# Kernel optimization log

Measured on AMD Instinct MI355X. Metric: run time of the kernel, lower is better.

The kernel has to match this reference:

```python
import jax, jax.numpy as jnp
import numpy as np

N_HEADS = 8
D_MODEL = 128
EPS = 1e-6


def setup_inputs() -> dict:
    key = jax.random.key(0)
    k1, k2, k3, k4, k5 = jax.random.split(key, 5)
    B, Dim, F, T = 1, D_MODEL, 256, 1024
    queries = jax.random.normal(k1, (B, Dim, F, T), dtype=jnp.float32)
    keys = jax.random.normal(k2, (B, Dim, F, T), dtype=jnp.float32)
    values = jax.random.normal(k3, (B, Dim, F, T), dtype=jnp.float32)
    # out_projection: Linear(d_model, d_output) with d_output == d_model
    W_out = jax.random.normal(k4, (D_MODEL, D_MODEL), dtype=jnp.float32) / np.sqrt(D_MODEL)
    b_out = jax.random.normal(k5, (D_MODEL,), dtype=jnp.float32) * 0.01
    return {"queries": queries, "keys": keys, "values": values,
            "W_out": W_out, "b_out": b_out}


def _to_heads(x, B, Dim, L, H):
    # (B, Dim, F, T) -> (B, L, Dim) -> (B, L, H, d) -> (B, H, L, d)
    return x.reshape(B, Dim, L).transpose(0, 2, 1).reshape(B, L, H, Dim // H).transpose(0, 2, 1, 3)


def reference(queries, keys, values, W_out, b_out):
    B, Dim, F, T = queries.shape
    L = F * T
    H = N_HEADS
    q = jax.nn.sigmoid(_to_heads(queries, B, Dim, L, H))  # (B,H,L,d)
    k = jax.nn.sigmoid(_to_heads(keys, B, Dim, L, H))
    v = _to_heads(values, B, Dim, L, H)

    # NOTE: sums are over the HEAD axis (dim=1), faithful to the original code
    ks = k.sum(axis=1, keepdims=True)                      # (B,1,L,d)
    qs = q.sum(axis=1, keepdims=True)
    sink_incoming = 1.0 / jnp.sum((q + EPS) * (ks + EPS), axis=-1)      # (B,H,L)
    source_outgoing = 1.0 / jnp.sum((k + EPS) * (qs + EPS), axis=-1)    # (B,H,L)
    conserved_sink = jnp.sum(
        (q + EPS) * ((k * source_outgoing[..., None]).sum(axis=1, keepdims=True) + EPS),
        axis=-1)                                                        # (B,H,L)
    conserved_source = jnp.sum(
        (k + EPS) * ((q * sink_incoming[..., None]).sum(axis=1, keepdims=True) + EPS),
        axis=-1)
    conserved_source = jnp.clip(conserved_source, -1.0, 1.0)
    sink_allocation = jax.nn.sigmoid(conserved_sink * (float(L) / float(L)))
    source_competition = jax.nn.softmax(conserved_source, axis=-1) * float(L)

    kv = jnp.einsum('bhld,bhlm->bhdm', k, v * source_competition[..., None])
    qkv = jnp.einsum('bhld,bhdm->bhlm', q * sink_incoming[..., None], kv)
    x = (qkv * sink_allocation[..., None]).transpose(0, 2, 1, 3).reshape(B, L, Dim)
    x = x @ W_out.T + b_out                                 # dropout is identity (eval)
    return x.transpose(0, 2, 1).reshape(B, Dim, F, T)
```

## Files before the change

kernel.cpp:

```cpp
#include <hip/hip_runtime.h>
#include <hip/hip_bf16.h>

#define L_TOT (1 << 18)
#define L_SHIFT 18
#define NHEAD 8
#define DHEAD 16
#define DMODEL 128
#define EPSF 1e-6f

typedef float f32x4 __attribute__((ext_vector_type(4)));
typedef short bf16x8 __attribute__((ext_vector_type(8)));

__device__ __forceinline__ float frcp(float x) { return __builtin_amdgcn_rcpf(x); }
__device__ __forceinline__ float sigm(float x) { return frcp(1.0f + __expf(-x)); }
__device__ __forceinline__ unsigned short f2bf(float f) {
    return (unsigned short)((__float_as_uint(f) + 0x8000u) >> 16);
}

__device__ __forceinline__ float qsum(float x) {
    x += __int_as_float(__builtin_amdgcn_update_dpp(0, __float_as_int(x), 0xB1, 0xf, 0xf, true));
    x += __int_as_float(__builtin_amdgcn_update_dpp(0, __float_as_int(x), 0x4E, 0xf, 0xf, true));
    return x;
}

__global__ __launch_bounds__(256) void k1_stats(
        const float* __restrict__ Q, const float* __restrict__ K,
        float* __restrict__ scale_o, float* __restrict__ wbuf,
        float* __restrict__ sep) {
    __shared__ float hredl[4][8];

    const int t = threadIdx.x;
    const int l0 = blockIdx.x * 64;
    const int c = t >> 2;
    const int s = t & 3;
    const int l = l0 + c;

    float qv[32], kv[32];
#pragma unroll
    for (int h = 0; h < 8; ++h)
#pragma unroll
        for (int r = 0; r < 4; ++r) {
            const int p = h * 16 + s * 4 + r;
            qv[h * 4 + r] = Q[(p << L_SHIFT) + l];
            kv[h * 4 + r] = K[(p << L_SHIFT) + l];
        }

    unsigned a[32];
#pragma unroll
    for (int i = 0; i < 32; ++i) {
        const unsigned qu = __float_as_uint(sigm(qv[i])) + 0x8000u;
        const unsigned ku = __float_as_uint(sigm(kv[i])) + 0x8000u;
        a[i] = (ku & 0xffff0000u) | (qu >> 16);
    }

    float ks[4] = {0.f, 0.f, 0.f, 0.f}, qs[4] = {0.f, 0.f, 0.f, 0.f};
#pragma unroll
    for (int h = 0; h < 8; ++h)
#pragma unroll
        for (int j = 0; j < 4; ++j) {
            const unsigned u = a[h * 4 + j];
            qs[j] += __uint_as_float(u << 16);
            ks[j] += __uint_as_float(u & 0xffff0000u);
        }

    float kse[4], qse[4];
#pragma unroll
    for (int j = 0; j < 4; ++j) { kse[j] = ks[j] + EPSF; qse[j] = qs[j] + EPSF; }

    float si[8], so[8];
#pragma unroll
    for (int h = 0; h < 8; ++h) {
        float aq = 0.f, ak = 0.f;
#pragma unroll
        for (int j = 0; j < 4; ++j) {
            const unsigned u = a[h * 4 + j];
            aq += (__uint_as_float(u << 16) + EPSF) * kse[j];
            ak += (__uint_as_float(u & 0xffff0000u) + EPSF) * qse[j];
        }
        si[h] = frcp(qsum(aq));
        so[h] = frcp(qsum(ak));
    }

    float kso[4] = {0.f, 0.f, 0.f, 0.f}, qsi[4] = {0.f, 0.f, 0.f, 0.f};
#pragma unroll
    for (int h = 0; h < 8; ++h)
#pragma unroll
        for (int j = 0; j < 4; ++j) {
            const unsigned u = a[h * 4 + j];
            kso[j] += __uint_as_float(u & 0xffff0000u) * so[h];
            qsi[j] += __uint_as_float(u << 16) * si[h];
        }
#pragma unroll
    for (int j = 0; j < 4; ++j) { kse[j] = kso[j] + EPSF; qse[j] = qsi[j] + EPSF; }

    float e2[2], sc2[2];
#pragma unroll
    for (int h = 0; h < 8; ++h) {
        float aq = 0.f, ak = 0.f;
#pragma unroll
        for (int j = 0; j < 4; ++j) {
            const unsigned u = a[h * 4 + j];
            aq += (__uint_as_float(u << 16) + EPSF) * kse[j];
            ak += (__uint_as_float(u & 0xffff0000u) + EPSF) * qse[j];
        }
        const float ck = qsum(aq);
        float cs = qsum(ak);
        if ((h >> 1) == s) {
            cs = fminf(fmaxf(cs, -1.f), 1.f);
            e2[h & 1] = __expf(cs);
            sc2[h & 1] = sigm(ck) * si[h];
        }
    }

    wbuf[((2 * s + 0) << L_SHIFT) + l] = e2[0];
    wbuf[((2 * s + 1) << L_SHIFT) + l] = e2[1];
    scale_o[((2 * s + 0) << L_SHIFT) + l] = sc2[0];
    scale_o[((2 * s + 1) << L_SHIFT) + l] = sc2[1];

    float v0 = e2[0], v1 = e2[1];
    v0 += __shfl_xor(v0, 4, 64);  v1 += __shfl_xor(v1, 4, 64);
    v0 += __shfl_xor(v0, 8, 64);  v1 += __shfl_xor(v1, 8, 64);
    v0 += __shfl_xor(v0, 16, 64); v1 += __shfl_xor(v1, 16, 64);
    v0 += __shfl_xor(v0, 32, 64); v1 += __shfl_xor(v1, 32, 64);
    if ((t & 63) < 4) {
        const int w = t >> 6;
        hredl[w][2 * s + 0] = v0;
        hredl[w][2 * s + 1] = v1;
    }
    __syncthreads();
    if (t < 8)
        sep[blockIdx.x * 8 + t] = hredl[0][t] + hredl[1][t] + hredl[2][t] + hredl[3][t];
}

__global__ __launch_bounds__(256) void k2_kv(
        const float* __restrict__ Kg, const float* __restrict__ Vg,
        const float* __restrict__ wg, float* __restrict__ parts) {
    const int b = blockIdx.x;
    const int h = b >> 6;
    const int blk = b & 63;
    const int t = threadIdx.x;
    const int dd = t >> 4, m = t & 15;

    __shared__ float A[16][132];
    __shared__ float Vv[16][132];
    __shared__ float wl[128];

    const int baseK = (h * DHEAD) << L_SHIFT;
    float acc = 0.f;

    for (int ch = 0; ch < 32; ++ch) {
        const int l0 = blk * 4096 + ch * 128;
        __syncthreads();
        if (t < 128) wl[t] = wg[(h << L_SHIFT) + l0 + t];
        __syncthreads();
#pragma unroll
        for (int i = 0; i < 2; ++i) {
            const int e = t + i * 256;
            const int r = e >> 5, c4 = e & 31;
            const float4 kq = *(const float4*)&Kg[baseK + (r << L_SHIFT) + l0 + c4 * 4];
            const float4 vq = *(const float4*)&Vg[baseK + (r << L_SHIFT) + l0 + c4 * 4];
            A[r][c4 * 4 + 0] = sigm(kq.x) * wl[c4 * 4 + 0];
            A[r][c4 * 4 + 1] = sigm(kq.y) * wl[c4 * 4 + 1];
            A[r][c4 * 4 + 2] = sigm(kq.z) * wl[c4 * 4 + 2];
            A[r][c4 * 4 + 3] = sigm(kq.w) * wl[c4 * 4 + 3];
            *(float4*)&Vv[r][c4 * 4] = vq;
        }
        __syncthreads();
#pragma unroll
        for (int c4 = 0; c4 < 32; ++c4) {
            const float4 av = *(const float4*)&A[dd][c4 * 4];
            const float4 vv = *(const float4*)&Vv[m][c4 * 4];
            acc += av.x * vv.x + av.y * vv.y + av.z * vv.z + av.w * vv.w;
        }
    }
    parts[b * 256 + t] = acc;
}

__global__ __launch_bounds__(256) void k3_wkv(
        const float* __restrict__ Wg, const float* __restrict__ parts,
        const float* __restrict__ sep, unsigned* __restrict__ wkvb) {
    const int hb = blockIdx.x;
    const int t = threadIdx.x;
    __shared__ float kvf[256];
    __shared__ float redl[4];

    float p = 0.f;
#pragma unroll
    for (int i = 0; i < 16; ++i) p += sep[(t + i * 256) * 8 + hb];
#pragma unroll
    for (int o = 32; o >= 1; o >>= 1) p += __shfl_xor(p, o, 64);
    if ((t & 63) == 0) redl[t >> 6] = p;

    float kacc = 0.f;
    for (int j = 0; j < 64; ++j)
        kacc += parts[(hb * 64 + j) * 256 + t];

    __syncthreads();
    const float s = (float)L_TOT / (redl[0] + redl[1] + redl[2] + redl[3]);
    kvf[t] = kacc * s;
    __syncthreads();

#pragma unroll
    for (int i = 0; i < 4; ++i) {
        const int j = t + i * 256;
        const int dim = j & 127, prp = j >> 7;
        float a0 = 0.f, a1 = 0.f;
#pragma unroll
        for (int mm = 0; mm < 16; ++mm) {
            const float wv = Wg[dim * 128 + hb * 16 + mm];
            a0 += wv * kvf[(2 * prp) * 16 + mm];
            a1 += wv * kvf[(2 * prp + 1) * 16 + mm];
        }
        wkvb[dim * 64 + hb * 8 + prp] = ((unsigned)f2bf(a1) << 16) | f2bf(a0);
    }
}

__global__ __launch_bounds__(256) void k4_mfma(
        const float* __restrict__ Q, const float* __restrict__ scale_g,
        const unsigned* __restrict__ wkvb, const float* __restrict__ bg,
        float* __restrict__ out) {
    __shared__ unsigned A_lds[128 * 68];
    __shared__ float bias[128];
    const int t = threadIdx.x;

#pragma unroll
    for (int i = 0; i < 8; ++i) {
        const int idx4 = t + i * 256;
        const uint4 v = ((const uint4*)wkvb)[idx4];
        const int row = idx4 >> 4, c4 = idx4 & 15;
        *(uint4*)&A_lds[row * 68 + c4 * 4] = v;
    }
    if (t < 128) bias[t] = bg[t];
    __syncthreads();

    const int w = t >> 6, lane = t & 63;
    const int lq = lane & 15, lh = lane >> 4;

#pragma unroll
    for (int ci = 0; ci < 2; ++ci) {
        const int l = blockIdx.x * 128 + ci * 64 + w * 16 + lq;

        float qv[4][8];
        float scv[4];
#pragma unroll
        for (int ks = 0; ks < 4; ++ks) {
            scv[ks] = scale_g[((ks * 2 + (lane >> 5)) << L_SHIFT) + l];
#pragma unroll
            for (int j = 0; j < 8; ++j) {
                const int p = ks * 32 + lh * 8 + j;
                qv[ks][j] = Q[(p << L_SHIFT) + l];
            }
        }
        bf16x8 bfr[4];
#pragma unroll
        for (int ks = 0; ks < 4; ++ks)
#pragma unroll
            for (int j = 0; j < 8; ++j)
                bfr[ks][j] = (short)f2bf(sigm(qv[ks][j]) * scv[ks]);

        f32x4 acc[8];
#pragma unroll
        for (int mt = 0; mt < 8; ++mt)
            acc[mt] = *(const f32x4*)&bias[mt * 16 + lh * 4];

#pragma unroll
        for (int ks = 0; ks < 4; ++ks) {
#pragma unroll
            for (int mt = 0; mt < 8; ++mt) {
                const int row = mt * 16 + lq;
                const bf16x8 aA = *(const bf16x8*)&A_lds[row * 68 + ks * 16 + lh * 4];
                acc[mt] = __builtin_amdgcn_mfma_f32_16x16x32_bf16(aA, bfr[ks], acc[mt], 0, 0, 0);
            }
        }

#pragma unroll
        for (int mt = 0; mt < 8; ++mt) {
#pragma unroll
            for (int r = 0; r < 4; ++r) {
                const int dim = mt * 16 + lh * 4 + r;
                out[(dim << L_SHIFT) + l] = acc[mt][r];
            }
        }
    }
}

extern "C" void kernel_launch(void* const* d_in, const int* in_sizes, int n_in,
                              void* d_out, int out_size, void* d_ws, size_t ws_size,
                              hipStream_t stream) {
    const float* Q = (const float*)d_in[0];
    const float* K = (const float*)d_in[1];
    const float* V = (const float*)d_in[2];
    const float* W = (const float*)d_in[3];
    const float* B = (const float*)d_in[4];
    float* out = (float*)d_out;
    float* ws = (float*)d_ws;

    float* parts    = ws;
    unsigned* wkvb  = (unsigned*)(ws + 131072);
    float* sep      = ws + 139264;
    float* scale    = ws + 172032;
    float* wbuf     = scale + 8 * L_TOT;

    k1_stats<<<L_TOT / 64, 256, 0, stream>>>(Q, K, scale, wbuf, sep);
    k2_kv<<<NHEAD * 64, 256, 0, stream>>>(K, V, wbuf, parts);
    k3_wkv<<<NHEAD, 256, 0, stream>>>(W, parts, sep, wkvb);
    k4_mfma<<<L_TOT / 128, 256, 0, stream>>>(Q, scale, wkvb, B, out);
}
```

Baseline: 222.1 us.

## Compute KV outer products with bf16 MFMA and drop EPS adds in stats

Rewrites the k2 K^T·V reduction to use 16x16x32 bf16 MFMA directly from global loads, replacing the shared-memory fp32 dot-product loop. The grid doubles to 1024 blocks, so the partial buffer and the k3 reduction double as well. Separately, k1 packs bf16 pairs with a single v_perm and drops the per-element +EPS on q and k in the normalizer sums. Both changes reduce ALU and LDS work, at the cost of bf16 rounding in KV and a small numerical deviation from the EPS terms.

```diff
diff --git a/kernel.cpp b/kernel.cpp
--- a/kernel.cpp
+++ b/kernel.cpp
@@ -50,7 +50,7 @@
     for (int i = 0; i < 32; ++i) {
         const unsigned qu = __float_as_uint(sigm(qv[i])) + 0x8000u;
         const unsigned ku = __float_as_uint(sigm(kv[i])) + 0x8000u;
-        a[i] = (ku & 0xffff0000u) | (qu >> 16);
+        a[i] = __builtin_amdgcn_perm(ku, qu, 0x07060302u);
     }
 
     float ks[4] = {0.f, 0.f, 0.f, 0.f}, qs[4] = {0.f, 0.f, 0.f, 0.f};
@@ -74,8 +74,8 @@
 #pragma unroll
         for (int j = 0; j < 4; ++j) {
             const unsigned u = a[h * 4 + j];
-            aq += (__uint_as_float(u << 16) + EPSF) * kse[j];
-            ak += (__uint_as_float(u & 0xffff0000u) + EPSF) * qse[j];
+            aq += __uint_as_float(u << 16) * kse[j];
+            ak += __uint_as_float(u & 0xffff0000u) * qse[j];
         }
         si[h] = frcp(qsum(aq));
         so[h] = frcp(qsum(ak));
@@ -100,8 +100,8 @@
 #pragma unroll
         for (int j = 0; j < 4; ++j) {
             const unsigned u = a[h * 4 + j];
-            aq += (__uint_as_float(u << 16) + EPSF) * kse[j];
-            ak += (__uint_as_float(u & 0xffff0000u) + EPSF) * qse[j];
+            aq += __uint_as_float(u << 16) * kse[j];
+            ak += __uint_as_float(u & 0xffff0000u) * qse[j];
         }
         const float ck = qsum(aq);
         float cs = qsum(ak);
@@ -135,45 +135,53 @@
 __global__ __launch_bounds__(256) void k2_kv(
         const float* __restrict__ Kg, const float* __restrict__ Vg,
         const float* __restrict__ wg, float* __restrict__ parts) {
+    __shared__ float kvred[4][256];
     const int b = blockIdx.x;
-    const int h = b >> 6;
-    const int blk = b & 63;
+    const int h = b >> 7;
+    const int blk = b & 127;
     const int t = threadIdx.x;
-    const int dd = t >> 4, m = t & 15;
-
-    __shared__ float A[16][132];
-    __shared__ float Vv[16][132];
-    __shared__ float wl[128];
-
-    const int baseK = (h * DHEAD) << L_SHIFT;
-    float acc = 0.f;
-
-    for (int ch = 0; ch < 32; ++ch) {
-        const int l0 = blk * 4096 + ch * 128;
-        __syncthreads();
-        if (t < 128) wl[t] = wg[(h << L_SHIFT) + l0 + t];
-        __syncthreads();
-#pragma unroll
-        for (int i = 0; i < 2; ++i) {
-            const int e = t + i * 256;
-            const int r = e >> 5, c4 = e & 31;
-            const float4 kq = *(const float4*)&Kg[baseK + (r << L_SHIFT) + l0 + c4 * 4];
-            const float4 vq = *(const float4*)&Vg[baseK + (r << L_SHIFT) + l0 + c4 * 4];
-            A[r][c4 * 4 + 0] = sigm(kq.x) * wl[c4 * 4 + 0];
-            A[r][c4 * 4 + 1] = sigm(kq.y) * wl[c4 * 4 + 1];
-            A[r][c4 * 4 + 2] = sigm(kq.z) * wl[c4 * 4 + 2];
-            A[r][c4 * 4 + 3] = sigm(kq.w) * wl[c4 * 4 + 3];
-            *(float4*)&Vv[r][c4 * 4] = vq;
-        }
-        __syncthreads();
-#pragma unroll
-        for (int c4 = 0; c4 < 32; ++c4) {
-            const float4 av = *(const float4*)&A[dd][c4 * 4];
-            const float4 vv = *(const float4*)&Vv[m][c4 * 4];
-            acc += av.x * vv.x + av.y * vv.y + av.z * vv.z + av.w * vv.w;
-        }
-    }
-    parts[b * 256 + t] = acc;
+    const int wv = t >> 6, lane = t & 63;
+    const int lq = lane & 15, lh = lane >> 4;
+
+    const int rowKV = ((h * DHEAD + lq) << L_SHIFT);
+    const int rowW  = (h << L_SHIFT);
+    const int lbase = blk * 2048 + wv * 512 + lh * 8;
+
+    f32x4 acc = {0.f, 0.f, 0.f, 0.f};
+#pragma unroll 4
+    for (int ch = 0; ch < 16; ++ch) {
+        const int lo = lbase + ch * 32;
+        const float4 ka = *(const float4*)&Kg[rowKV + lo];
+        const float4 kb = *(const float4*)&Kg[rowKV + lo + 4];
+        const float4 va = *(const float4*)&Vg[rowKV + lo];
+        const float4 vb = *(const float4*)&Vg[rowKV + lo + 4];
+        const float4 wa = *(const float4*)&wg[rowW + lo];
+        const float4 wb = *(const float4*)&wg[rowW + lo + 4];
+        bf16x8 af, bvf;
+        af[0] = (short)f2bf(sigm(ka.x) * wa.x);
+        af[1] = (short)f2bf(sigm(ka.y) * wa.y);
+        af[2] = (short)f2bf(sigm(ka.z) * wa.z);
+        af[3] = (short)f2bf(sigm(ka.w) * wa.w);
+        af[4] = (short)f2bf(sigm(kb.x) * wb.x);
+        af[5] = (short)f2bf(sigm(kb.y) * wb.y);
+        af[6] = (short)f2bf(sigm(kb.z) * wb.z);
+        af[7] = (short)f2bf(sigm(kb.w) * wb.w);
+        bvf[0] = (short)f2bf(va.x);
+        bvf[1] = (short)f2bf(va.y);
+        bvf[2] = (short)f2bf(va.z);
+        bvf[3] = (short)f2bf(va.w);
+        bvf[4] = (short)f2bf(vb.x);
+        bvf[5] = (short)f2bf(vb.y);
+        bvf[6] = (short)f2bf(vb.z);
+        bvf[7] = (short)f2bf(vb.w);
+        acc = __builtin_amdgcn_mfma_f32_16x16x32_bf16(af, bvf, acc, 0, 0, 0);
+    }
+
+#pragma unroll
+    for (int r = 0; r < 4; ++r)
+        kvred[wv][(lh * 4 + r) * 16 + lq] = acc[r];
+    __syncthreads();
+    parts[b * 256 + t] = kvred[0][t] + kvred[1][t] + kvred[2][t] + kvred[3][t];
 }
 
 __global__ __launch_bounds__(256) void k3_wkv(
@@ -192,8 +200,8 @@
     if ((t & 63) == 0) redl[t >> 6] = p;
 
     float kacc = 0.f;
-    for (int j = 0; j < 64; ++j)
-        kacc += parts[(hb * 64 + j) * 256 + t];
+    for (int j = 0; j < 128; ++j)
+        kacc += parts[(hb * 128 + j) * 256 + t];
 
     __syncthreads();
     const float s = (float)L_TOT / (redl[0] + redl[1] + redl[2] + redl[3]);
@@ -296,13 +304,13 @@
     float* ws = (float*)d_ws;
 
     float* parts    = ws;
-    unsigned* wkvb  = (unsigned*)(ws + 131072);
-    float* sep      = ws + 139264;
-    float* scale    = ws + 172032;
+    unsigned* wkvb  = (unsigned*)(ws + 262144);
+    float* sep      = ws + 270336;
+    float* scale    = ws + 303104;
     float* wbuf     = scale + 8 * L_TOT;
 
     k1_stats<<<L_TOT / 64, 256, 0, stream>>>(Q, K, scale, wbuf, sep);
-    k2_kv<<<NHEAD * 64, 256, 0, stream>>>(K, V, wbuf, parts);
+    k2_kv<<<NHEAD * 128, 256, 0, stream>>>(K, V, wbuf, parts);
     k3_wkv<<<NHEAD, 256, 0, stream>>>(W, parts, sep, wkvb);
     k4_mfma<<<L_TOT / 128, 256, 0, stream>>>(Q, scale, wkvb, B, out);
 }
```

Result: faster. 190.6 us (-14.2%).
